# Optimization experiments

Measured on AMD Instinct MI355X. Metric: run time of the kernel, lower is better.

## Reference

```python
import jax, jax.numpy as jnp
import numpy as np

MB, T, NP1, D, K = 512, 256, 201, 4, 5
CTX = D + 4  # context_dim = amp_dim + 4


def setup_inputs() -> dict:
    key = jax.random.key(0)
    ks = jax.random.split(key, 10)
    demands = jax.random.uniform(ks[0], (MB, NP1)) * 9.0 + 1.0
    demands = demands.at[:, 0].set(0.0)  # depot has zero demand
    coords = jax.random.uniform(ks[1], (MB, NP1, 2))
    psi_prime = jax.random.normal(ks[2], (MB, NP1, D))
    knn_indices = jax.random.randint(ks[3], (MB, NP1, K), 0, NP1)
    actions = jax.random.randint(ks[4], (MB, T), 0, NP1)
    Wq_w = jax.random.normal(ks[5], (D, CTX)) * 0.1
    Wq_b = jax.random.normal(ks[6], (D,)) * 0.1
    return {
        'demands': demands, 'coords': coords, 'psi_prime': psi_prime,
        'Wq_w': Wq_w, 'Wq_b': Wq_b,
        'lambda_param': jnp.float32(0.1), 'mu_param': jnp.float32(0.5),
        'nu_param': jnp.float32(0.1),
        'actions': actions, 'knn_indices': knn_indices, 'capacity': 50,
    }


def _forward(demands, coords, psi_prime, Wq_w, Wq_b,
             lambda_param, mu_param, nu_param,
             actions, knn_indices, capacity):
    mb, T = actions.shape
    np1 = psi_prime.shape[1]
    n_customers = np1 - 1
    cap = max(float(capacity), 1e-8)
    b_idx = jnp.arange(mb)

    # --- sequential state bookkeeping (cur node, used capacity, visited mask) ---
    def step(carry, act_t):
        cur, used, vis = carry
        out = (cur, used, vis)  # state BEFORE applying action t
        at_depot = act_t == 0
        dem_t = demands[b_idx, act_t]
        used_n = jnp.where(at_depot, 0.0, used + dem_t)
        vis_n = vis.at[b_idx, act_t].set(True).at[:, 0].set(False)
        return (act_t, used_n, vis_n), out

    init = (jnp.zeros(mb, jnp.int32), jnp.zeros(mb, demands.dtype),
            jnp.zeros((mb, np1), bool))
    _, (all_cur, all_used, all_vis) = jax.lax.scan(step, init,
                                                   actions.T.astype(jnp.int32))
    all_cur = all_cur.T                       # [mb,T]
    all_used = all_used.T                     # [mb,T]
    all_vis = jnp.transpose(all_vis, (1, 0, 2))  # [mb,T,np1]

    remaining = cap - all_used
    cap_norm = remaining / cap
    exceeds = demands[:, None, :] > remaining[:, :, None]   # [mb,T,np1]
    mask = (all_vis | exceeds).at[:, :, 0].set(False)
    at_depot3 = all_cur == 0
    has_cust = (~mask[:, :, 1:]).any(-1)
    mask = mask.at[:, :, 0].set(at_depot3 & has_cust)

    cur_coords = coords[b_idx[:, None], all_cur]            # [mb,T,2]
    psi_curr = psi_prime[b_idx[:, None], all_cur]           # [mb,T,D]
    psi_curr = jnp.where(at_depot3[..., None], 0.0, psi_curr)
    t_norm = jnp.broadcast_to(
        (jnp.arange(T, dtype=psi_prime.dtype) / max(n_customers, 1))[None, :],
        (mb, T))
    ctx = jnp.concatenate([psi_curr, cap_norm[..., None],
                           t_norm[..., None], cur_coords], -1)  # [mb,T,D+4]
    query = ctx @ Wq_w.T + Wq_b                              # [mb,T,D]
    context_scores = jnp.einsum('btd,bnd->btn', query, psi_prime)

    # kNN interference: psi is fixed over t, so compute once and broadcast
    neigh = psi_prime[b_idx[:, None, None], knn_indices]     # [mb,np1,K,D]
    interference = jnp.einsum('bnd,bnkd->bn', psi_prime, neigh)  # [mb,np1]

    diff = coords[:, None, :, :] - cur_coords[:, :, None, :]  # [mb,T,np1,2]
    dist = jnp.sqrt(jnp.sum(diff * diff, -1) + 1e-12)         # [mb,T,np1]

    mu = jnp.clip(mu_param, 0.0, 20.0)
    lam = jnp.clip(lambda_param, -2.0, 3.0)
    nu = jnp.clip(nu_param, -2.0, 3.0)
    scores = (context_scores + lam * interference[:, None, :]
              - mu * dist + nu * (demands[:, None, :] / cap))
    scores = jnp.where(mask, -1e9, scores)
    lp3 = jax.nn.log_softmax(scores, -1)                      # [mb,T,np1]
    lp_new = jnp.take_along_axis(lp3, actions[:, :, None], 2)[..., 0]
    entropy = (-(jnp.exp(lp3) * lp3).sum(-1)).mean(1)         # [mb]
    return lp_new, entropy


def reference(demands, coords, psi_prime, Wq_w, Wq_b,
              lambda_param, mu_param, nu_param,
              actions, knn_indices, capacity):
    return _forward(demands, coords, psi_prime, Wq_w, Wq_b,
                    lambda_param, mu_param, nu_param,
                    actions, knn_indices, capacity)
```

## Files before the change

### kernel.cpp

```cpp
#include <hip/hip_runtime.h>
#include <hip/hip_bf16.h>
#include <math.h>

#define MB 512
#define T 256
#define NP1 201
#define KNN 5

typedef unsigned long long u64;
typedef unsigned int u32;

__global__ __launch_bounds__(256, 2) void fused_kernel(
        const float* __restrict__ demands,
        const float* __restrict__ coords,
        const float* __restrict__ psi,
        const float* __restrict__ Wq_w,
        const float* __restrict__ Wq_b,
        const float* __restrict__ lam_p,
        const float* __restrict__ mu_p,
        const float* __restrict__ nu_p,
        const int* __restrict__ actions,
        const int* __restrict__ knn,
        const int* __restrict__ cap_p,
        float* __restrict__ lp_out,
        float* __restrict__ ent_out) {
    __shared__ float4 psiL[NP1];
    __shared__ float4 zCL[NP1];
    __shared__ u64   visW[4][T];
    __shared__ float remL[T];
    __shared__ int   actL[T];
    __shared__ float demL[T];
    __shared__ u64   aggV[4][4];
    __shared__ int   aggD[4];
    __shared__ float entPart[4];

    const int b = blockIdx.x;
    const int tid = threadIdx.x;
    const int lane = tid & 63, wv = tid >> 6;

    const float cap = fmaxf((float)cap_p[0], 1e-8f);

    const int t = tid;
    const int a_t = actions[b * T + t];
    actL[t] = a_t;
    demL[t] = demands[b * NP1 + a_t];

    u64 m0 = (a_t < 64)                ? (1ull << a_t)         : 0ull;
    u64 m1 = (a_t >= 64 && a_t < 128)  ? (1ull << (a_t - 64))  : 0ull;
    u64 m2 = (a_t >= 128 && a_t < 192) ? (1ull << (a_t - 128)) : 0ull;
    u64 m3 = (a_t >= 192)              ? (1ull << (a_t - 192)) : 0ull;
    int d = (a_t == 0) ? t : -1;

    float4 packP, packC;
    if (t < NP1) {
        const float lam = fminf(fmaxf(lam_p[0], -2.f), 3.f);
        const float nu  = fminf(fmaxf(nu_p[0],  -2.f), 3.f);
        const float4 pn = *(const float4*)(psi + ((size_t)b * NP1 + t) * 4);
        const float2 cc2 = *(const float2*)(coords + ((size_t)b * NP1 + t) * 2);
        float interf = 0.f;
        const int* kn = knn + ((size_t)b * NP1 + t) * KNN;
#pragma unroll
        for (int k = 0; k < KNN; ++k) {
            const int j = kn[k];
            const float4 pj = *(const float4*)(psi + ((size_t)b * NP1 + j) * 4);
            interf += pn.x * pj.x + pn.y * pj.y + pn.z * pj.z + pn.w * pj.w;
        }
        const float dem = demands[b * NP1 + t];
        packP = pn;
        packC.x = lam * interf + nu * (dem / cap);
        packC.y = cc2.x; packC.z = cc2.y; packC.w = dem;
    }

#pragma unroll
    for (int off = 1; off < 64; off <<= 1) {
        m0 |= __shfl_up(m0, off);
        m1 |= __shfl_up(m1, off);
        m2 |= __shfl_up(m2, off);
        m3 |= __shfl_up(m3, off);
        d = max(d, __shfl_up(d, off));
    }
    if (lane == 63) {
        aggV[0][wv] = m0; aggV[1][wv] = m1;
        aggV[2][wv] = m2; aggV[3][wv] = m3;
        aggD[wv] = d;
    }
    __syncthreads();

    u64 p0 = 0, p1 = 0, p2 = 0, p3 = 0; int pd = -1;
    for (int u = 0; u < wv; ++u) {
        p0 |= aggV[0][u]; p1 |= aggV[1][u];
        p2 |= aggV[2][u]; p3 |= aggV[3][u];
        pd = max(pd, aggD[u]);
    }
    m0 |= p0; m1 |= p1; m2 |= p2; m3 |= p3; d = max(d, pd);
    visW[0][t] = m0; visW[1][t] = m1; visW[2][t] = m2; visW[3][t] = m3;

    int dPrev = __shfl_up(d, 1);
    if (lane == 0) dPrev = pd;
    const int s = dPrev + 1;

    float used = 0.f;
    for (int j = s; j < t; ++j) used += demL[j];
    remL[t] = cap - used;

    if (t < NP1) { psiL[t] = packP; zCL[t] = packC; }
    __syncthreads();

    const int rloc = tid >> 2, split = tid & 3;
    const float mu  = fminf(fmaxf(mu_p[0], 0.f), 20.f);

    const int base = 1 + split * 50;
    const int wsel = base >> 6;
    const int woff = base & 63;

    float q0[4], q1[4], q2[4], q3[4], ccx[4], ccy[4], remA[4];
    u64 window[4];
    bool adep[4];
#pragma unroll
    for (int c = 0; c < 4; ++c) {
        const int tr = c * 64 + rloc;
        const float rem = remL[tr];
        remA[c] = rem;
        const int cur = (tr == 0) ? 0 : actL[tr - 1];
        const bool at_depot = (cur == 0);
        adep[c] = at_depot;

        u64 wlo = 0, whi = 0;
        if (tr > 0) {
            wlo = visW[wsel][tr - 1];
            whi = (wsel < 3) ? visW[wsel + 1][tr - 1] : 0ull;
        }
        window[c] = (wlo >> woff) | (whi << (64 - woff));

        float4 pc = psiL[cur];
        if (at_depot) { pc.x = 0.f; pc.y = 0.f; pc.z = 0.f; pc.w = 0.f; }
        const float4 cz = zCL[cur];
        ccx[c] = cz.y; ccy[c] = cz.z;

        const float capn = rem / cap;
        const float tn = (float)tr / 200.f;
        const float c0 = pc.x, c1 = pc.y, c2 = pc.z, c3 = pc.w;
        q0[c] = Wq_b[0] + Wq_w[0]*c0 + Wq_w[1]*c1 + Wq_w[2]*c2 + Wq_w[3]*c3
              + Wq_w[4]*capn + Wq_w[5]*tn + Wq_w[6]*ccx[c] + Wq_w[7]*ccy[c];
        q1[c] = Wq_b[1] + Wq_w[8]*c0 + Wq_w[9]*c1 + Wq_w[10]*c2 + Wq_w[11]*c3
              + Wq_w[12]*capn + Wq_w[13]*tn + Wq_w[14]*ccx[c] + Wq_w[15]*ccy[c];
        q2[c] = Wq_b[2] + Wq_w[16]*c0 + Wq_w[17]*c1 + Wq_w[18]*c2 + Wq_w[19]*c3
              + Wq_w[20]*capn + Wq_w[21]*tn + Wq_w[22]*ccx[c] + Wq_w[23]*ccy[c];
        q3[c] = Wq_b[3] + Wq_w[24]*c0 + Wq_w[25]*c1 + Wq_w[26]*c2 + Wq_w[27]*c3
              + Wq_w[28]*capn + Wq_w[29]*tn + Wq_w[30]*ccx[c] + Wq_w[31]*ccy[c];
    }

    float S[4] = {0.f, 0.f, 0.f, 0.f};
    float W[4] = {0.f, 0.f, 0.f, 0.f};
#pragma unroll 5
    for (int i = 0; i < 50; ++i) {
        const int n = base + i;
        const float4 p4 = psiL[n];
        const float4 c4 = zCL[n];
#pragma unroll
        for (int c = 0; c < 4; ++c) {
            float sco = fmaf(q0[c], p4.x, fmaf(q1[c], p4.y,
                        fmaf(q2[c], p4.z, fmaf(q3[c], p4.w, c4.x))));
            const float dx = c4.y - ccx[c], dy = c4.z - ccy[c];
            sco = fmaf(-mu, __builtin_amdgcn_sqrtf(fmaf(dx, dx, fmaf(dy, dy, 1e-12f))), sco);
            const bool maskn = (((u32)(window[c] >> i)) & 1u) || (c4.w > remA[c]);
            const float e = maskn ? 0.f : __expf(sco);
            S[c] += e;
            W[c] = fmaf(e, sco, W[c]);
        }
    }

#pragma unroll
    for (int c = 0; c < 4; ++c) {
        S[c] += __shfl_xor(S[c], 1); S[c] += __shfl_xor(S[c], 2);
        W[c] += __shfl_xor(W[c], 1); W[c] += __shfl_xor(W[c], 2);
    }

    float entv = 0.f;
    if (split == 0) {
        const float4 pD = psiL[0];
        const float4 zD = zCL[0];
#pragma unroll
        for (int c = 0; c < 4; ++c) {
            const int tr = c * 64 + rloc;
            const bool hasCust = S[c] > 0.f;
            {
                float sco = fmaf(q0[c], pD.x, fmaf(q1[c], pD.y,
                            fmaf(q2[c], pD.z, fmaf(q3[c], pD.w, zD.x))));
                const float dx = zD.y - ccx[c], dy = zD.z - ccy[c];
                sco = fmaf(-mu, __builtin_amdgcn_sqrtf(fmaf(dx, dx, fmaf(dy, dy, 1e-12f))), sco);
                const bool mk = adep[c] && hasCust;
                const float e = mk ? 0.f : __expf(sco);
                S[c] += e;
                W[c] = fmaf(e, sco, W[c]);
            }
            const float L = __logf(S[c]);
            const int a_row = actL[tr];
            const float4 p4 = psiL[a_row];
            const float4 c4 = zCL[a_row];
            float sco = fmaf(q0[c], p4.x, fmaf(q1[c], p4.y,
                        fmaf(q2[c], p4.z, fmaf(q3[c], p4.w, c4.x))));
            const float dx = c4.y - ccx[c], dy = c4.z - ccy[c];
            sco = fmaf(-mu, __builtin_amdgcn_sqrtf(fmaf(dx, dx, fmaf(dy, dy, 1e-12f))), sco);
            bool maskA;
            if (a_row == 0) {
                maskA = adep[c] && hasCust;
            } else {
                const u64 vw = (tr > 0) ? visW[a_row >> 6][tr - 1] : 0ull;
                maskA = ((vw >> (a_row & 63)) & 1ull) || (c4.w > remA[c]);
            }
            const float sAct = maskA ? -1e9f : sco;
            lp_out[b * T + tr] = sAct - L;
            entv += L - W[c] / S[c];
        }
    }

#pragma unroll
    for (int o = 32; o > 0; o >>= 1) entv += __shfl_xor(entv, o);
    if (lane == 0) entPart[wv] = entv;
    __syncthreads();
    if (tid == 0)
        ent_out[b] = (entPart[0] + entPart[1] + entPart[2] + entPart[3])
                     * (1.f / (float)T);
}

extern "C" void kernel_launch(void* const* d_in, const int* in_sizes, int n_in,
                              void* d_out, int out_size, void* d_ws, size_t ws_size,
                              hipStream_t stream) {
    const float* demands = (const float*)d_in[0];
    const float* coords  = (const float*)d_in[1];
    const float* psi     = (const float*)d_in[2];
    const float* Wq_w    = (const float*)d_in[3];
    const float* Wq_b    = (const float*)d_in[4];
    const float* lam_p   = (const float*)d_in[5];
    const float* mu_p    = (const float*)d_in[6];
    const float* nu_p    = (const float*)d_in[7];
    const int*   actions = (const int*)d_in[8];
    const int*   knn     = (const int*)d_in[9];
    const int*   cap_p   = (const int*)d_in[10];

    float* lp_out  = (float*)d_out;
    float* ent_out = lp_out + MB * T;

    (void)d_ws; (void)ws_size;

    fused_kernel<<<MB, 256, 0, stream>>>(
        demands, coords, psi, Wq_w, Wq_b, lam_p, mu_p, nu_p,
        actions, knn, cap_p, lp_out, ent_out);
}
```

Baseline: 103.5 us.

## Double block size and split prologue work across two thread halves

Result: faster. 101.4 us (-2.1%).

```diff
diff --git a/kernel.cpp b/kernel.cpp
--- a/kernel.cpp
+++ b/kernel.cpp
@@ -10,7 +10,7 @@
 typedef unsigned long long u64;
 typedef unsigned int u32;
 
-__global__ __launch_bounds__(256, 2) void fused_kernel(
+__global__ __launch_bounds__(512, 4) void fused_kernel(
         const float* __restrict__ demands,
         const float* __restrict__ coords,
         const float* __restrict__ psi,
@@ -32,7 +32,7 @@
     __shared__ float demL[T];
     __shared__ u64   aggV[4][4];
     __shared__ int   aggD[4];
-    __shared__ float entPart[4];
+    __shared__ float entPart[8];
 
     const int b = blockIdx.x;
     const int tid = threadIdx.x;
@@ -40,70 +40,77 @@
 
     const float cap = fmaxf((float)cap_p[0], 1e-8f);
 
-    const int t = tid;
-    const int a_t = actions[b * T + t];
-    actL[t] = a_t;
-    demL[t] = demands[b * NP1 + a_t];
-
-    u64 m0 = (a_t < 64)                ? (1ull << a_t)         : 0ull;
-    u64 m1 = (a_t >= 64 && a_t < 128)  ? (1ull << (a_t - 64))  : 0ull;
-    u64 m2 = (a_t >= 128 && a_t < 192) ? (1ull << (a_t - 128)) : 0ull;
-    u64 m3 = (a_t >= 192)              ? (1ull << (a_t - 192)) : 0ull;
-    int d = (a_t == 0) ? t : -1;
-
-    float4 packP, packC;
-    if (t < NP1) {
-        const float lam = fminf(fmaxf(lam_p[0], -2.f), 3.f);
-        const float nu  = fminf(fmaxf(nu_p[0],  -2.f), 3.f);
-        const float4 pn = *(const float4*)(psi + ((size_t)b * NP1 + t) * 4);
-        const float2 cc2 = *(const float2*)(coords + ((size_t)b * NP1 + t) * 2);
-        float interf = 0.f;
-        const int* kn = knn + ((size_t)b * NP1 + t) * KNN;
-#pragma unroll
-        for (int k = 0; k < KNN; ++k) {
-            const int j = kn[k];
-            const float4 pj = *(const float4*)(psi + ((size_t)b * NP1 + j) * 4);
-            interf += pn.x * pj.x + pn.y * pj.y + pn.z * pj.z + pn.w * pj.w;
-        }
-        const float dem = demands[b * NP1 + t];
-        packP = pn;
-        packC.x = lam * interf + nu * (dem / cap);
-        packC.y = cc2.x; packC.z = cc2.y; packC.w = dem;
-    }
-
-#pragma unroll
-    for (int off = 1; off < 64; off <<= 1) {
-        m0 |= __shfl_up(m0, off);
-        m1 |= __shfl_up(m1, off);
-        m2 |= __shfl_up(m2, off);
-        m3 |= __shfl_up(m3, off);
-        d = max(d, __shfl_up(d, off));
-    }
-    if (lane == 63) {
-        aggV[0][wv] = m0; aggV[1][wv] = m1;
-        aggV[2][wv] = m2; aggV[3][wv] = m3;
-        aggD[wv] = d;
+    u64 m0 = 0, m1 = 0, m2 = 0, m3 = 0;
+    int d = -1;
+    if (tid < T) {
+        const int t = tid;
+        const int a_t = actions[b * T + t];
+        actL[t] = a_t;
+        demL[t] = demands[b * NP1 + a_t];
+
+        m0 = (a_t < 64)                ? (1ull << a_t)         : 0ull;
+        m1 = (a_t >= 64 && a_t < 128)  ? (1ull << (a_t - 64))  : 0ull;
+        m2 = (a_t >= 128 && a_t < 192) ? (1ull << (a_t - 128)) : 0ull;
+        m3 = (a_t >= 192)              ? (1ull << (a_t - 192)) : 0ull;
+        d = (a_t == 0) ? t : -1;
+
+#pragma unroll
+        for (int off = 1; off < 64; off <<= 1) {
+            m0 |= __shfl_up(m0, off);
+            m1 |= __shfl_up(m1, off);
+            m2 |= __shfl_up(m2, off);
+            m3 |= __shfl_up(m3, off);
+            d = max(d, __shfl_up(d, off));
+        }
+        if (lane == 63) {
+            aggV[0][wv] = m0; aggV[1][wv] = m1;
+            aggV[2][wv] = m2; aggV[3][wv] = m3;
+            aggD[wv] = d;
+        }
+    } else {
+        const int t2 = tid - T;
+        if (t2 < NP1) {
+            const float lam = fminf(fmaxf(lam_p[0], -2.f), 3.f);
+            const float nu  = fminf(fmaxf(nu_p[0],  -2.f), 3.f);
+            const float4 pn = *(const float4*)(psi + ((size_t)b * NP1 + t2) * 4);
+            const float2 cc2 = *(const float2*)(coords + ((size_t)b * NP1 + t2) * 2);
+            float interf = 0.f;
+            const int* kn = knn + ((size_t)b * NP1 + t2) * KNN;
+#pragma unroll
+            for (int k = 0; k < KNN; ++k) {
+                const int j = kn[k];
+                const float4 pj = *(const float4*)(psi + ((size_t)b * NP1 + j) * 4);
+                interf += pn.x * pj.x + pn.y * pj.y + pn.z * pj.z + pn.w * pj.w;
+            }
+            const float dem = demands[b * NP1 + t2];
+            float4 packC;
+            packC.x = lam * interf + nu * (dem / cap);
+            packC.y = cc2.x; packC.z = cc2.y; packC.w = dem;
+            psiL[t2] = pn;
+            zCL[t2] = packC;
+        }
     }
     __syncthreads();
 
-    u64 p0 = 0, p1 = 0, p2 = 0, p3 = 0; int pd = -1;
-    for (int u = 0; u < wv; ++u) {
-        p0 |= aggV[0][u]; p1 |= aggV[1][u];
-        p2 |= aggV[2][u]; p3 |= aggV[3][u];
-        pd = max(pd, aggD[u]);
-    }
-    m0 |= p0; m1 |= p1; m2 |= p2; m3 |= p3; d = max(d, pd);
-    visW[0][t] = m0; visW[1][t] = m1; visW[2][t] = m2; visW[3][t] = m3;
-
-    int dPrev = __shfl_up(d, 1);
-    if (lane == 0) dPrev = pd;
-    const int s = dPrev + 1;
-
-    float used = 0.f;
-    for (int j = s; j < t; ++j) used += demL[j];
-    remL[t] = cap - used;
-
-    if (t < NP1) { psiL[t] = packP; zCL[t] = packC; }
+    if (tid < T) {
+        const int t = tid;
+        u64 p0 = 0, p1 = 0, p2 = 0, p3 = 0; int pd = -1;
+        for (int u = 0; u < wv; ++u) {
+            p0 |= aggV[0][u]; p1 |= aggV[1][u];
+            p2 |= aggV[2][u]; p3 |= aggV[3][u];
+            pd = max(pd, aggD[u]);
+        }
+        m0 |= p0; m1 |= p1; m2 |= p2; m3 |= p3; d = max(d, pd);
+        visW[0][t] = m0; visW[1][t] = m1; visW[2][t] = m2; visW[3][t] = m3;
+
+        int dPrev = __shfl_up(d, 1);
+        if (lane == 0) dPrev = pd;
+        const int s = dPrev + 1;
+
+        float used = 0.f;
+        for (int j = s; j < t; ++j) used += demL[j];
+        remL[t] = cap - used;
+    }
     __syncthreads();
 
     const int rloc = tid >> 2, split = tid & 3;
@@ -113,12 +120,12 @@
     const int wsel = base >> 6;
     const int woff = base & 63;
 
-    float q0[4], q1[4], q2[4], q3[4], ccx[4], ccy[4], remA[4];
-    u64 window[4];
-    bool adep[4];
-#pragma unroll
-    for (int c = 0; c < 4; ++c) {
-        const int tr = c * 64 + rloc;
+    float q0[2], q1[2], q2[2], q3[2], ccx[2], ccy[2], remA[2];
+    u64 window[2];
+    bool adep[2];
+#pragma unroll
+    for (int c = 0; c < 2; ++c) {
+        const int tr = c * 128 + rloc;
         const float rem = remL[tr];
         remA[c] = rem;
         const int cur = (tr == 0) ? 0 : actL[tr - 1];
@@ -150,15 +157,15 @@
               + Wq_w[28]*capn + Wq_w[29]*tn + Wq_w[30]*ccx[c] + Wq_w[31]*ccy[c];
     }
 
-    float S[4] = {0.f, 0.f, 0.f, 0.f};
-    float W[4] = {0.f, 0.f, 0.f, 0.f};
+    float S[2] = {0.f, 0.f};
+    float W[2] = {0.f, 0.f};
 #pragma unroll 5
     for (int i = 0; i < 50; ++i) {
         const int n = base + i;
         const float4 p4 = psiL[n];
         const float4 c4 = zCL[n];
 #pragma unroll
-        for (int c = 0; c < 4; ++c) {
+        for (int c = 0; c < 2; ++c) {
             float sco = fmaf(q0[c], p4.x, fmaf(q1[c], p4.y,
                         fmaf(q2[c], p4.z, fmaf(q3[c], p4.w, c4.x))));
             const float dx = c4.y - ccx[c], dy = c4.z - ccy[c];
@@ -171,7 +178,7 @@
     }
 
 #pragma unroll
-    for (int c = 0; c < 4; ++c) {
+    for (int c = 0; c < 2; ++c) {
         S[c] += __shfl_xor(S[c], 1); S[c] += __shfl_xor(S[c], 2);
         W[c] += __shfl_xor(W[c], 1); W[c] += __shfl_xor(W[c], 2);
     }
@@ -181,8 +188,8 @@
         const float4 pD = psiL[0];
         const float4 zD = zCL[0];
 #pragma unroll
-        for (int c = 0; c < 4; ++c) {
-            const int tr = c * 64 + rloc;
+        for (int c = 0; c < 2; ++c) {
+            const int tr = c * 128 + rloc;
             const bool hasCust = S[c] > 0.f;
             {
                 float sco = fmaf(q0[c], pD.x, fmaf(q1[c], pD.y,
@@ -219,9 +226,12 @@
     for (int o = 32; o > 0; o >>= 1) entv += __shfl_xor(entv, o);
     if (lane == 0) entPart[wv] = entv;
     __syncthreads();
-    if (tid == 0)
-        ent_out[b] = (entPart[0] + entPart[1] + entPart[2] + entPart[3])
-                     * (1.f / (float)T);
+    if (tid == 0) {
+        float tot = 0.f;
+#pragma unroll
+        for (int u = 0; u < 8; ++u) tot += entPart[u];
+        ent_out[b] = tot * (1.f / (float)T);
+    }
 }
 
 extern "C" void kernel_launch(void* const* d_in, const int* in_sizes, int n_in,
@@ -244,7 +254,7 @@
 
     (void)d_ws; (void)ws_size;
 
-    fused_kernel<<<MB, 256, 0, stream>>>(
+    fused_kernel<<<MB, 512, 0, stream>>>(
         demands, coords, psi, Wq_w, Wq_b, lam_p, mu_p, nu_p,
         actions, knn, cap_p, lp_out, ent_out);
 }
```
